# Kernel tuning notes

Hardware: AMD Instinct MI355X
Metric: run time of the kernel (lower is better)

Reference implementation:

```python
import jax, jax.numpy as jnp
import numpy as np

BATCH, NBITS = 32768, 512


def setup_inputs() -> dict:
    key = jax.random.key(0)
    raw = jax.random.randint(key, (BATCH, NBITS), 0, 2)
    bits = raw.astype(jnp.float32) * 2.0 - 1.0  # values in {-1, +1}
    return {"bits": bits}


def _joint_prob(b):
    # b in {0,1}, shape [B, N]. p_ij[i,j,m,n] = mean_b 1[b_i==m] * 1[b_j==n]
    B = b.shape[0]
    ind = jnp.stack([(b == 0.0), (b == 1.0)], axis=0).astype(b.dtype)  # [2, B, N]
    return jnp.einsum('mbi,nbj->ijmn', ind, ind) / B  # [N, N, 2, 2]


def reference(bits):
    b = bits / 2.0 + 0.5
    N = b.shape[1]
    p_ij = _joint_prob(b)
    p_i_pos = b.mean(axis=0)
    p_i = jnp.stack([1.0 - p_i_pos, p_i_pos], axis=-1)  # [N, 2]
    outer = p_i[:, None, :, None] * p_i[None, :, None, :]  # [N, N, 2, 2]
    ii = jnp.arange(N)
    tri = (ii[:, None] > ii[None, :])[:, :, None, None]  # triangle: keep i > j
    valid = tri & (p_ij > 0) & (p_i[:, None, :, None] > 0) & (p_i[None, :, None, :] > 0)
    safe_p = jnp.where(valid, p_ij, 1.0)
    safe_o = jnp.where(valid, outer, 1.0)
    terms = jnp.where(valid, safe_p * jnp.log(safe_p / safe_o), 0.0)
    cnt = valid.sum().astype(bits.dtype)
    return terms.sum() / cnt
```

## Files before the change

### kernel.cpp

```cpp
#include <hip/hip_runtime.h>
#include <stdint.h>

#define BATCH   32768
#define NBITS   512
#define NWORDS  512
#define NPAIRS  130816
#define NSLICE  7
#define CH      37

typedef unsigned long long u64;

__global__ __launch_bounds__(256) void pack_kernel(const float* __restrict__ bits,
                                                   u64* __restrict__ packed,
                                                   int* __restrict__ C,
                                                   double* __restrict__ lg) {
    const int gid = blockIdx.x * 256 + threadIdx.x;

    reinterpret_cast<int4*>(C)[gid] = make_int4(0, 0, 0, 0);

    if (gid <= BATCH) lg[gid] = (gid > 0) ? log((double)gid) : 0.0;

    const int wv   = threadIdx.x >> 6;
    const int lane = threadIdx.x & 63;
    const int gw   = blockIdx.x * 4 + wv;
    const int cg   = gw & 1;
    const int w    = gw >> 1;
    const int c0   = cg * 256 + lane * 4;

    u64 m0 = 0, m1 = 0, m2 = 0, m3 = 0;
    const float* base = bits + (size_t)w * 64 * NBITS + c0;
#pragma unroll 16
    for (int r = 0; r < 64; ++r) {
        float4 v = *reinterpret_cast<const float4*>(base + (size_t)r * NBITS);
        const u64 b = 1ull << r;
        if (v.x > 0.0f) m0 |= b;
        if (v.y > 0.0f) m1 |= b;
        if (v.z > 0.0f) m2 |= b;
        if (v.w > 0.0f) m3 |= b;
    }
    u64* dst = packed + (size_t)w * NBITS + c0;
    dst[0] = m0; dst[1] = m1; dst[2] = m2; dst[3] = m3;
}

__global__ __launch_bounds__(256) void gram_kernel(const u64* __restrict__ packed,
                                                   int* __restrict__ C) {
    __shared__ u64 ldsI[CH][64];
    __shared__ u64 ldsJ[CH][64];

    const int s = blockIdx.x % NSLICE;
    const int t = blockIdx.x / NSLICE;
    int bi = (int)((sqrtf(8.0f * (float)t + 1.0f) - 1.0f) * 0.5f);
    while ((bi + 1) * (bi + 2) / 2 <= t) ++bi;
    while (bi * (bi + 1) / 2 > t) --bi;
    const int bj = t - bi * (bi + 1) / 2;

    const int i0 = bi * 64, j0 = bj * 64;
    const int w0 = (s * NWORDS) / NSLICE;
    const int w1 = ((s + 1) * NWORDS) / NSLICE;
    const bool diag = (bi == bj);

    const int ti2 = (threadIdx.x & 15) * 2;
    const int tj2 = (threadIdx.x >> 4) * 2;

    int acc[4][4] = {};

    for (int wb = w0; wb < w1; wb += CH) {
        const int nw = min(CH, w1 - wb);
        __syncthreads();
        for (int q = threadIdx.x; q < nw * 32; q += 256) {
            const int wo = q >> 5, cp = (q & 31) * 2;
            const size_t g = (size_t)(wb + wo) * NBITS;
            *reinterpret_cast<ulonglong2*>(&ldsI[wo][cp]) =
                *reinterpret_cast<const ulonglong2*>(&packed[g + i0 + cp]);
            if (!diag)
                *reinterpret_cast<ulonglong2*>(&ldsJ[wo][cp]) =
                    *reinterpret_cast<const ulonglong2*>(&packed[g + j0 + cp]);
        }
        __syncthreads();
        const u64 (*BJ)[64] = diag ? ldsI : ldsJ;
#pragma unroll 2
        for (int w = 0; w < nw; ++w) {
            const u64 a0 = ldsI[w][ti2],      a1 = ldsI[w][ti2 + 1];
            const u64 a2 = ldsI[w][ti2 + 32], a3 = ldsI[w][ti2 + 33];
            const u64 b0 = BJ[w][tj2],        b1 = BJ[w][tj2 + 1];
            const u64 b2 = BJ[w][tj2 + 32],   b3 = BJ[w][tj2 + 33];
            acc[0][0] += __popcll(a0 & b0); acc[0][1] += __popcll(a0 & b1);
            acc[0][2] += __popcll(a0 & b2); acc[0][3] += __popcll(a0 & b3);
            acc[1][0] += __popcll(a1 & b0); acc[1][1] += __popcll(a1 & b1);
            acc[1][2] += __popcll(a1 & b2); acc[1][3] += __popcll(a1 & b3);
            acc[2][0] += __popcll(a2 & b0); acc[2][1] += __popcll(a2 & b1);
            acc[2][2] += __popcll(a2 & b2); acc[2][3] += __popcll(a2 & b3);
            acc[3][0] += __popcll(a3 & b0); acc[3][1] += __popcll(a3 & b1);
            acc[3][2] += __popcll(a3 & b2); acc[3][3] += __popcll(a3 & b3);
        }
    }

    const int ic[4] = {i0 + ti2, i0 + ti2 + 1, i0 + ti2 + 32, i0 + ti2 + 33};
    const int jc[4] = {j0 + tj2, j0 + tj2 + 1, j0 + tj2 + 32, j0 + tj2 + 33};
#pragma unroll
    for (int a = 0; a < 4; ++a)
#pragma unroll
        for (int b = 0; b < 4; ++b)
            atomicAdd(&C[(size_t)ic[a] * NBITS + jc[b]], acc[a][b]);
}

__global__ __launch_bounds__(256) void mi_kernel(const int* __restrict__ C,
                                                 const double* __restrict__ lg,
                                                 double* __restrict__ bsum,
                                                 int* __restrict__ bcnt) {
    const double invB = 1.0 / (double)BATCH;
    double lsum = 0.0;
    int lcnt = 0;

    const int k = blockIdx.x * 256 + threadIdx.x;
    if (k < NPAIRS) {
        int i = (int)((1.0 + sqrt(1.0 + 8.0 * (double)k)) * 0.5);
        while ((i * (i - 1)) / 2 > k) --i;
        while (((i + 1) * i) / 2 <= k) ++i;
        const int j = k - (i * (i - 1)) / 2;

        const int n11 = C[i * NBITS + j];
        const int ci  = C[i * NBITS + i];
        const int cj  = C[j * NBITS + j];

        const int pim[2] = {BATCH - ci, ci};
        const int pjn[2] = {BATCH - cj, cj};
        const int nmn[2][2] = {{BATCH - ci - cj + n11, cj - n11},
                               {ci - n11, n11}};
        const double lgB = lg[BATCH];

#pragma unroll
        for (int m = 0; m < 2; ++m)
#pragma unroll
            for (int n = 0; n < 2; ++n) {
                const int c_mn = nmn[m][n];
                if (c_mn > 0 && pim[m] > 0 && pjn[n] > 0) {
                    lsum += (double)c_mn * invB *
                            (lg[c_mn] + lgB - lg[pim[m]] - lg[pjn[n]]);
                    ++lcnt;
                }
            }
    }

    __shared__ double ssum[256];
    __shared__ int scnt[256];
    ssum[threadIdx.x] = lsum;
    scnt[threadIdx.x] = lcnt;
    __syncthreads();
    for (int off = 128; off > 0; off >>= 1) {
        if (threadIdx.x < off) {
            ssum[threadIdx.x] += ssum[threadIdx.x + off];
            scnt[threadIdx.x] += scnt[threadIdx.x + off];
        }
        __syncthreads();
    }
    if (threadIdx.x == 0) { bsum[blockIdx.x] = ssum[0]; bcnt[blockIdx.x] = scnt[0]; }
}

__global__ __launch_bounds__(256) void final_kernel(const double* __restrict__ bsum,
                                                    const int* __restrict__ bcnt,
                                                    float* __restrict__ out,
                                                    int nblocks) {
    __shared__ double ssum[256];
    __shared__ int scnt[256];
    double s = 0.0; int c = 0;
    for (int k = threadIdx.x; k < nblocks; k += 256) { s += bsum[k]; c += bcnt[k]; }
    ssum[threadIdx.x] = s;
    scnt[threadIdx.x] = c;
    __syncthreads();
    for (int off = 128; off > 0; off >>= 1) {
        if (threadIdx.x < off) {
            ssum[threadIdx.x] += ssum[threadIdx.x + off];
            scnt[threadIdx.x] += scnt[threadIdx.x + off];
        }
        __syncthreads();
    }
    if (threadIdx.x == 0) out[0] = (float)(ssum[0] / (double)scnt[0]);
}

extern "C" void kernel_launch(void* const* d_in, const int* in_sizes, int n_in,
                              void* d_out, int out_size, void* d_ws, size_t ws_size,
                              hipStream_t stream) {
    const float* bits = (const float*)d_in[0];
    char* ws = (char*)d_ws;
    u64*    packed = (u64*)ws;
    int*    C      = (int*)(ws + (2u << 20));
    double* lg     = (double*)(ws + (3u << 20));
    double* bsum   = (double*)(ws + (3u << 20) + 524288);
    int*    bcnt   = (int*)(ws + (3u << 20) + 524288 + 8192);

    pack_kernel<<<256, 256, 0, stream>>>(bits, packed, C, lg);
    gram_kernel<<<36 * NSLICE, 256, 0, stream>>>(packed, C);
    mi_kernel<<<512, 256, 0, stream>>>(C, lg, bsum, bcnt);
    final_kernel<<<1, 256, 0, stream>>>(bsum, bcnt, (float*)d_out, 512);
}
```

Before: 51.59 us.

## Replace atomic Gram accumulation with per-slice partial buffers and row-based MI

```diff
diff --git a/kernel.cpp b/kernel.cpp
--- a/kernel.cpp
+++ b/kernel.cpp
@@ -4,19 +4,16 @@
 #define BATCH   32768
 #define NBITS   512
 #define NWORDS  512
-#define NPAIRS  130816
-#define NSLICE  7
-#define CH      37
+#define NSLICE  16
+#define SW      32
+#define NTILE   36
 
 typedef unsigned long long u64;
 
 __global__ __launch_bounds__(256) void pack_kernel(const float* __restrict__ bits,
                                                    u64* __restrict__ packed,
-                                                   int* __restrict__ C,
                                                    double* __restrict__ lg) {
     const int gid = blockIdx.x * 256 + threadIdx.x;
-
-    reinterpret_cast<int4*>(C)[gid] = make_int4(0, 0, 0, 0);
 
     if (gid <= BATCH) lg[gid] = (gid > 0) ? log((double)gid) : 0.0;
 
@@ -43,103 +40,106 @@
 }
 
 __global__ __launch_bounds__(256) void gram_kernel(const u64* __restrict__ packed,
-                                                   int* __restrict__ C) {
-    __shared__ u64 ldsI[CH][64];
-    __shared__ u64 ldsJ[CH][64];
+                                                   int* __restrict__ Cp) {
+    __shared__ u64 ldsI[SW][64];
+    __shared__ u64 ldsJ[SW][64];
 
-    const int s = blockIdx.x % NSLICE;
-    const int t = blockIdx.x / NSLICE;
+    const int s = blockIdx.x & (NSLICE - 1);
+    const int t = blockIdx.x >> 4;
     int bi = (int)((sqrtf(8.0f * (float)t + 1.0f) - 1.0f) * 0.5f);
     while ((bi + 1) * (bi + 2) / 2 <= t) ++bi;
     while (bi * (bi + 1) / 2 > t) --bi;
     const int bj = t - bi * (bi + 1) / 2;
 
     const int i0 = bi * 64, j0 = bj * 64;
-    const int w0 = (s * NWORDS) / NSLICE;
-    const int w1 = ((s + 1) * NWORDS) / NSLICE;
+    const int w0 = s * SW;
     const bool diag = (bi == bj);
+
+    for (int q = threadIdx.x; q < SW * 32; q += 256) {
+        const int wo = q >> 5, cp = (q & 31) * 2;
+        const size_t g = (size_t)(w0 + wo) * NBITS;
+        *reinterpret_cast<ulonglong2*>(&ldsI[wo][cp]) =
+            *reinterpret_cast<const ulonglong2*>(&packed[g + i0 + cp]);
+        if (!diag)
+            *reinterpret_cast<ulonglong2*>(&ldsJ[wo][cp]) =
+                *reinterpret_cast<const ulonglong2*>(&packed[g + j0 + cp]);
+    }
+    __syncthreads();
 
     const int ti2 = (threadIdx.x & 15) * 2;
     const int tj2 = (threadIdx.x >> 4) * 2;
+    const u64 (*BJ)[64] = diag ? ldsI : ldsJ;
 
     int acc[4][4] = {};
-
-    for (int wb = w0; wb < w1; wb += CH) {
-        const int nw = min(CH, w1 - wb);
-        __syncthreads();
-        for (int q = threadIdx.x; q < nw * 32; q += 256) {
-            const int wo = q >> 5, cp = (q & 31) * 2;
-            const size_t g = (size_t)(wb + wo) * NBITS;
-            *reinterpret_cast<ulonglong2*>(&ldsI[wo][cp]) =
-                *reinterpret_cast<const ulonglong2*>(&packed[g + i0 + cp]);
-            if (!diag)
-                *reinterpret_cast<ulonglong2*>(&ldsJ[wo][cp]) =
-                    *reinterpret_cast<const ulonglong2*>(&packed[g + j0 + cp]);
-        }
-        __syncthreads();
-        const u64 (*BJ)[64] = diag ? ldsI : ldsJ;
-#pragma unroll 2
-        for (int w = 0; w < nw; ++w) {
-            const u64 a0 = ldsI[w][ti2],      a1 = ldsI[w][ti2 + 1];
-            const u64 a2 = ldsI[w][ti2 + 32], a3 = ldsI[w][ti2 + 33];
-            const u64 b0 = BJ[w][tj2],        b1 = BJ[w][tj2 + 1];
-            const u64 b2 = BJ[w][tj2 + 32],   b3 = BJ[w][tj2 + 33];
-            acc[0][0] += __popcll(a0 & b0); acc[0][1] += __popcll(a0 & b1);
-            acc[0][2] += __popcll(a0 & b2); acc[0][3] += __popcll(a0 & b3);
-            acc[1][0] += __popcll(a1 & b0); acc[1][1] += __popcll(a1 & b1);
-            acc[1][2] += __popcll(a1 & b2); acc[1][3] += __popcll(a1 & b3);
-            acc[2][0] += __popcll(a2 & b0); acc[2][1] += __popcll(a2 & b1);
-            acc[2][2] += __popcll(a2 & b2); acc[2][3] += __popcll(a2 & b3);
-            acc[3][0] += __popcll(a3 & b0); acc[3][1] += __popcll(a3 & b1);
-            acc[3][2] += __popcll(a3 & b2); acc[3][3] += __popcll(a3 & b3);
-        }
+#pragma unroll 4
+    for (int w = 0; w < SW; ++w) {
+        const u64 a0 = ldsI[w][ti2],      a1 = ldsI[w][ti2 + 1];
+        const u64 a2 = ldsI[w][ti2 + 32], a3 = ldsI[w][ti2 + 33];
+        const u64 b0 = BJ[w][tj2],        b1 = BJ[w][tj2 + 1];
+        const u64 b2 = BJ[w][tj2 + 32],   b3 = BJ[w][tj2 + 33];
+        acc[0][0] += __popcll(a0 & b0); acc[0][1] += __popcll(a0 & b1);
+        acc[0][2] += __popcll(a0 & b2); acc[0][3] += __popcll(a0 & b3);
+        acc[1][0] += __popcll(a1 & b0); acc[1][1] += __popcll(a1 & b1);
+        acc[1][2] += __popcll(a1 & b2); acc[1][3] += __popcll(a1 & b3);
+        acc[2][0] += __popcll(a2 & b0); acc[2][1] += __popcll(a2 & b1);
+        acc[2][2] += __popcll(a2 & b2); acc[2][3] += __popcll(a2 & b3);
+        acc[3][0] += __popcll(a3 & b0); acc[3][1] += __popcll(a3 & b1);
+        acc[3][2] += __popcll(a3 & b2); acc[3][3] += __popcll(a3 & b3);
     }
 
+    int* out = Cp + (size_t)s * NBITS * NBITS;
     const int ic[4] = {i0 + ti2, i0 + ti2 + 1, i0 + ti2 + 32, i0 + ti2 + 33};
     const int jc[4] = {j0 + tj2, j0 + tj2 + 1, j0 + tj2 + 32, j0 + tj2 + 33};
 #pragma unroll
     for (int a = 0; a < 4; ++a)
 #pragma unroll
         for (int b = 0; b < 4; ++b)
-            atomicAdd(&C[(size_t)ic[a] * NBITS + jc[b]], acc[a][b]);
+            out[(size_t)ic[a] * NBITS + jc[b]] = acc[a][b];
 }
 
-__global__ __launch_bounds__(256) void mi_kernel(const int* __restrict__ C,
+__global__ __launch_bounds__(256) void mi_kernel(const int* __restrict__ Cp,
                                                  const double* __restrict__ lg,
                                                  double* __restrict__ bsum,
                                                  int* __restrict__ bcnt) {
     const double invB = 1.0 / (double)BATCH;
+    const int i = blockIdx.x;
     double lsum = 0.0;
     int lcnt = 0;
 
-    const int k = blockIdx.x * 256 + threadIdx.x;
-    if (k < NPAIRS) {
-        int i = (int)((1.0 + sqrt(1.0 + 8.0 * (double)k)) * 0.5);
-        while ((i * (i - 1)) / 2 > k) --i;
-        while (((i + 1) * i) / 2 <= k) ++i;
-        const int j = k - (i * (i - 1)) / 2;
-
-        const int n11 = C[i * NBITS + j];
-        const int ci  = C[i * NBITS + i];
-        const int cj  = C[j * NBITS + j];
-
-        const int pim[2] = {BATCH - ci, ci};
-        const int pjn[2] = {BATCH - cj, cj};
-        const int nmn[2][2] = {{BATCH - ci - cj + n11, cj - n11},
-                               {ci - n11, n11}};
-        const double lgB = lg[BATCH];
+    int ci = 0;
+#pragma unroll
+    for (int s = 0; s < NSLICE; ++s)
+        ci += Cp[(size_t)s * NBITS * NBITS + (size_t)i * NBITS + i];
 
 #pragma unroll
-        for (int m = 0; m < 2; ++m)
+    for (int half = 0; half < 2; ++half) {
+        const int j = half * 256 + threadIdx.x;
+        if (j < i) {
+            int n11 = 0, cj = 0;
 #pragma unroll
-            for (int n = 0; n < 2; ++n) {
-                const int c_mn = nmn[m][n];
-                if (c_mn > 0 && pim[m] > 0 && pjn[n] > 0) {
-                    lsum += (double)c_mn * invB *
-                            (lg[c_mn] + lgB - lg[pim[m]] - lg[pjn[n]]);
-                    ++lcnt;
+            for (int s = 0; s < NSLICE; ++s) {
+                const int* base = Cp + (size_t)s * NBITS * NBITS;
+                n11 += base[(size_t)i * NBITS + j];
+                cj  += base[(size_t)j * NBITS + j];
+            }
+
+            const int pim[2] = {BATCH - ci, ci};
+            const int pjn[2] = {BATCH - cj, cj};
+            const int nmn[2][2] = {{BATCH - ci - cj + n11, cj - n11},
+                                   {ci - n11, n11}};
+            const double lgB = lg[BATCH];
+#pragma unroll
+            for (int m = 0; m < 2; ++m)
+#pragma unroll
+                for (int n = 0; n < 2; ++n) {
+                    const int c_mn = nmn[m][n];
+                    if (c_mn > 0 && pim[m] > 0 && pjn[n] > 0) {
+                        lsum += (double)c_mn * invB *
+                                (lg[c_mn] + lgB - lg[pim[m]] - lg[pjn[n]]);
+                        ++lcnt;
+                    }
                 }
-            }
+        }
     }
 
     __shared__ double ssum[256];
@@ -184,13 +184,13 @@
     const float* bits = (const float*)d_in[0];
     char* ws = (char*)d_ws;
     u64*    packed = (u64*)ws;
-    int*    C      = (int*)(ws + (2u << 20));
-    double* lg     = (double*)(ws + (3u << 20));
-    double* bsum   = (double*)(ws + (3u << 20) + 524288);
-    int*    bcnt   = (int*)(ws + (3u << 20) + 524288 + 8192);
+    int*    Cp     = (int*)(ws + (2u << 20));
+    double* lg     = (double*)(ws + (18u << 20));
+    double* bsum   = (double*)(ws + (19u << 20));
+    int*    bcnt   = (int*)(ws + (19u << 20) + 8192);
 
-    pack_kernel<<<256, 256, 0, stream>>>(bits, packed, C, lg);
-    gram_kernel<<<36 * NSLICE, 256, 0, stream>>>(packed, C);
-    mi_kernel<<<512, 256, 0, stream>>>(C, lg, bsum, bcnt);
-    final_kernel<<<1, 256, 0, stream>>>(bsum, bcnt, (float*)d_out, 512);
+    pack_kernel<<<256, 256, 0, stream>>>(bits, packed, lg);
+    gram_kernel<<<NTILE * NSLICE, 256, 0, stream>>>(packed, Cp);
+    mi_kernel<<<NBITS, 256, 0, stream>>>(Cp, lg, bsum, bcnt);
+    final_kernel<<<1, 256, 0, stream>>>(bsum, bcnt, (float*)d_out, NBITS);
 }
```

Measured after the change: 54.86 us. 1.06x slower.
